# Kernel optimization log

Measured on AMD Instinct MI355X. Metric: run time of the kernel, lower is better.

The kernel has to match this reference:

```python
import jax, jax.numpy as jnp
import numpy as np

SEQ_LEN = 512
MAX_SPAN = 15
BATCH = 8
HIDDEN = 1024
WIDTH_DIM = 64
NUM_LABELS = 3


def _enumerate_spans(seq_len, max_span):
    starts, ends = [], []
    for s in range(seq_len):
        for e in range(s, min(s + max_span, seq_len)):
            starts.append(s)
            ends.append(e)
    return np.asarray(starts, np.int32), np.asarray(ends, np.int32)


def setup_inputs() -> dict:
    key = jax.random.key(0)
    k = jax.random.split(key, 6)
    starts, ends = _enumerate_spans(SEQ_LEN, MAX_SPAN)  # N = 7575
    d_in = HIDDEN * 2 + WIDTH_DIM  # 2112
    return {
        "sequence_output": jax.random.normal(k[0], (BATCH, SEQ_LEN, HIDDEN), jnp.float32),
        "width_emb": jax.random.normal(k[1], (MAX_SPAN, WIDTH_DIM), jnp.float32) * 0.02,
        "W1": jax.random.normal(k[2], (d_in, HIDDEN), jnp.float32) * (1.0 / np.sqrt(d_in)),
        "b1": jnp.zeros((HIDDEN,), jnp.float32),
        "W2": jax.random.normal(k[3], (HIDDEN, NUM_LABELS), jnp.float32) * (1.0 / np.sqrt(HIDDEN)),
        "b2": jnp.zeros((NUM_LABELS,), jnp.float32),
        "span_starts": jnp.asarray(starts),
        "span_ends": jnp.asarray(ends),
    }


def reference(sequence_output, width_emb, W1, b1, W2, b2, span_starts, span_ends):
    # Gather start/end token representations for every candidate span.
    B = sequence_output.shape[0]
    N = span_starts.shape[0]
    start_repr = sequence_output[:, span_starts]            # [B, N, H]
    end_repr = sequence_output[:, span_ends]                # [B, N, H]
    width_repr = width_emb[span_ends - span_starts]         # [N, 64]
    width_repr = jnp.broadcast_to(width_repr[None], (B, N, width_repr.shape[-1]))
    span_reprs = jnp.concatenate([start_repr, end_repr, width_repr], axis=-1)  # [B, N, 2H+64]
    # Span classifier MLP (dropout is identity in eval mode).
    h = jax.nn.relu(jnp.einsum("bnd,dh->bnh", span_reprs, W1) + b1)
    logits = jnp.einsum("bnh,hl->bnl", h, W2) + b2          # [B, N, num_labels]
    return logits
```

## Files before the change

kernel.cpp:

```cpp
#include <hip/hip_runtime.h>
#include <stdint.h>

#define SEQ 512
#define BATCH 8
#define HID 1024

typedef __attribute__((ext_vector_type(8))) __bf16 bf16x8;
typedef __attribute__((ext_vector_type(4))) float f32x4;

__device__ __forceinline__ unsigned short f2bf(float f) {
    unsigned int u = __float_as_uint(f);
    unsigned int r = 0x7fffu + ((u >> 16) & 1u);
    return (unsigned short)((u + r) >> 16);
}

__device__ __forceinline__ void unpack8(uint4 v, float* f) {
    f[0] = __uint_as_float(v.x << 16);
    f[1] = __uint_as_float(v.x & 0xffff0000u);
    f[2] = __uint_as_float(v.y << 16);
    f[3] = __uint_as_float(v.y & 0xffff0000u);
    f[4] = __uint_as_float(v.z << 16);
    f[5] = __uint_as_float(v.z & 0xffff0000u);
    f[6] = __uint_as_float(v.w << 16);
    f[7] = __uint_as_float(v.w & 0xffff0000u);
}

template <int CTRL>
__device__ __forceinline__ float dpp_add(float x) {
    int t = __builtin_amdgcn_update_dpp(0, __float_as_int(x), CTRL, 0xf, 0xf, true);
    return x + __int_as_float(t);
}
__device__ __forceinline__ float wave_sum63(float x) {
    x = dpp_add<0x111>(x);
    x = dpp_add<0x112>(x);
    x = dpp_add<0x114>(x);
    x = dpp_add<0x118>(x);
    x = dpp_add<0x142>(x);
    x = dpp_add<0x143>(x);
    return x;
}

__global__ __launch_bounds__(256) void k_prep(const float* __restrict__ seq,
                                              const float* __restrict__ wemb,
                                              const float* __restrict__ W1,
                                              const float* __restrict__ b1,
                                              const float* __restrict__ W2,
                                              ushort* __restrict__ seqb,
                                              ushort* __restrict__ Bt,
                                              ushort* __restrict__ Rbf,
                                              float* __restrict__ W2t) {
    __shared__ float tile[32][33];
    const int bid = blockIdx.x;
    const int tid = threadIdx.x;
    if (bid < 60) {
        int idx = bid * 256 + tid;
        int w = idx >> 10, j = idx & 1023;
        float a0 = b1[j], a1 = 0.f, a2 = 0.f, a3 = 0.f;
#pragma unroll
        for (int c = 0; c < 64; c += 4) {
            a0 = fmaf(wemb[w * 64 + c + 0], W1[(size_t)(2048 + c + 0) * 1024 + j], a0);
            a1 = fmaf(wemb[w * 64 + c + 1], W1[(size_t)(2048 + c + 1) * 1024 + j], a1);
            a2 = fmaf(wemb[w * 64 + c + 2], W1[(size_t)(2048 + c + 2) * 1024 + j], a2);
            a3 = fmaf(wemb[w * 64 + c + 3], W1[(size_t)(2048 + c + 3) * 1024 + j], a3);
        }
        Rbf[idx] = f2bf((a0 + a1) + (a2 + a3));
    } else if (bid < 72) {
        int idx = (bid - 60) * 256 + tid;
        int l = idx >> 10, j = idx & 1023;
        W2t[idx] = W2[j * 3 + l];
    } else if (bid < 4168) {
        int i = (bid - 72) * 256 + tid;
        float4 v = ((const float4*)seq)[i];
        ushort4 o;
        o.x = f2bf(v.x); o.y = f2bf(v.y); o.z = f2bf(v.z); o.w = f2bf(v.w);
        ((ushort4*)seqb)[i] = o;
    } else {
        int idx = bid - 4168;
        int nb = (idx & 63) * 32, kb = (idx >> 6) * 32;
        int tx = tid & 31, ty = tid >> 5;
        int n = nb + tx;
        int rb = (n < 1024) ? 0 : 1024;
        int nc = n - rb;
#pragma unroll
        for (int i = 0; i < 4; ++i) {
            int k = kb + ty + i * 8;
            tile[ty + i * 8][tx] = W1[(size_t)(rb + k) * 1024 + nc];
        }
        __syncthreads();
#pragma unroll
        for (int i = 0; i < 4; ++i) {
            int n2 = nb + ty + i * 8;
            Bt[(size_t)n2 * 1024 + kb + tx] = f2bf(tile[tx][ty + i * 8]);
        }
    }
}

__global__ __launch_bounds__(256) void k_gemm(const ushort* __restrict__ A,
                                              const ushort* __restrict__ Bt,
                                              ushort* __restrict__ P,
                                              ushort* __restrict__ Q) {
    __shared__ ushort Al[2][8192];
    __shared__ ushort Bl[2][8192];
    const int tid = threadIdx.x;
    const int wid = tid >> 6;
    const int lane = tid & 63;
    const int bid = blockIdx.x;
    const int x = bid & 7, t8 = bid >> 3;
    const int m0 = (((x >> 1) << 3) + (t8 >> 3)) * 128;
    const int n0 = (((x & 1) << 3) + (t8 & 7)) * 128;
    const int wm = (wid >> 1) * 64;
    const int wn = (wid & 1) * 64;
    const int srow = lane >> 2;
    const int scol = (lane & 3) * 8;
    const int fr = lane & 15;
    const int fk = (lane >> 4) * 8;

    f32x4 acc[4][4] = {};

    const ushort* Abase = A  + (size_t)(m0 + srow) * 1024 + scol;
    const ushort* Bbase = Bt + (size_t)(n0 + srow) * 1024 + scol;

#define STAGE(buf, k0)                                                                     \
    {                                                                                      \
        _Pragma("unroll")                                                                  \
        for (int r = 0; r < 4; ++r) {                                                      \
            int c = wid + 4 * r;                                                           \
            int half = c >> 3;                                                             \
            int rows = (c & 7) * 16;                                                       \
            const ushort* sa = Abase + (size_t)rows * 1024 + (k0) + half * 32;             \
            const ushort* sb = Bbase + (size_t)rows * 1024 + (k0) + half * 32;             \
            int loff = half * 4096 + rows * 32;                                            \
            __builtin_amdgcn_global_load_lds((const __attribute__((address_space(1))) void*)sa, \
                                             (__attribute__((address_space(3))) void*)(&Al[buf][loff]), \
                                             16, 0, 0);                                    \
            __builtin_amdgcn_global_load_lds((const __attribute__((address_space(1))) void*)sb, \
                                             (__attribute__((address_space(3))) void*)(&Bl[buf][loff]), \
                                             16, 0, 0);                                    \
        }                                                                                  \
    }

#define COMPUTE(cur)                                                                       \
    {                                                                                      \
        _Pragma("unroll")                                                                  \
        for (int kk = 0; kk < 2; ++kk) {                                                   \
            bf16x8 af[4], bg[4];                                                           \
            _Pragma("unroll")                                                              \
            for (int i = 0; i < 4; ++i)                                                    \
                af[i] = *(const bf16x8*)(&Al[cur][kk * 4096 + (wm + i * 16 + fr) * 32 + fk]); \
            _Pragma("unroll")                                                              \
            for (int j = 0; j < 4; ++j)                                                    \
                bg[j] = *(const bf16x8*)(&Bl[cur][kk * 4096 + (wn + j * 16 + fr) * 32 + fk]); \
            __builtin_amdgcn_s_setprio(1);                                                 \
            _Pragma("unroll")                                                              \
            for (int i = 0; i < 4; ++i)                                                    \
                _Pragma("unroll")                                                          \
                for (int j = 0; j < 4; ++j)                                                \
                    acc[i][j] = __builtin_amdgcn_mfma_f32_16x16x32_bf16(af[i], bg[j], acc[i][j], 0, 0, 0); \
            __builtin_amdgcn_s_setprio(0);                                                 \
        }                                                                                  \
    }

    STAGE(0, 0);
    for (int t = 0; t < 15; ++t) {
        const int cur = t & 1;
        STAGE(cur ^ 1, (t + 1) * 64);
        asm volatile("s_waitcnt vmcnt(8)" ::: "memory");
        __builtin_amdgcn_s_barrier();
        COMPUTE(cur);
        __builtin_amdgcn_s_barrier();
    }
    asm volatile("s_waitcnt vmcnt(0)" ::: "memory");
    __builtin_amdgcn_s_barrier();
    COMPUTE(1);
#undef STAGE
#undef COMPUTE

    ushort* Cb = (n0 < 1024) ? P : Q;
    const int nc0 = n0 & 1023;
    const int cr = (lane >> 4) * 4;
    const int cc = lane & 15;
#pragma unroll
    for (int i = 0; i < 4; ++i)
#pragma unroll
        for (int j = 0; j < 4; ++j) {
            ushort* Cp = Cb + (size_t)(m0 + wm + i * 16 + cr) * 1024 + (nc0 + wn + j * 16 + cc);
#pragma unroll
            for (int r = 0; r < 4; ++r)
                Cp[(size_t)r * 1024] = f2bf(acc[i][j][r]);
        }
}

__global__ __launch_bounds__(512, 2) void k_span6(const ushort* __restrict__ Pmat,
                                                  const ushort* __restrict__ Qmat,
                                                  const ushort* __restrict__ Rbf,
                                                  const float* __restrict__ W2t,
                                                  const float* __restrict__ b2,
                                                  float* __restrict__ out, int nspans) {
    __shared__ ushort Qs[22 * 1024];
    __shared__ ushort Rs[15 * 1024];
    const int tid = threadIdx.x;
    const int wid = tid >> 6, lane = tid & 63;
    const int b = blockIdx.x >> 6;
    const int s0 = (blockIdx.x & 63) << 3;

#pragma unroll
    for (int i = 0; i < 6; ++i) {
        int c = wid + (i << 3);
        if (c < 44) {
            int g = (c << 9) + lane * 8;
            int row = s0 + (g >> 10);
            if (row > SEQ - 1) row = SEQ - 1;
            const ushort* src = Qmat + (((size_t)(b << 9) + row) << 10) + (g & 1023);
            __builtin_amdgcn_global_load_lds((const __attribute__((address_space(1))) void*)src,
                                             (__attribute__((address_space(3))) void*)(Qs + (c << 9)),
                                             16, 0, 0);
        }
    }
#pragma unroll
    for (int i = 0; i < 4; ++i) {
        int c = wid + (i << 3);
        if (c < 30) {
            int g = (c << 9) + lane * 8;
            __builtin_amdgcn_global_load_lds((const __attribute__((address_space(1))) void*)(Rbf + g),
                                             (__attribute__((address_space(3))) void*)(Rs + (c << 9)),
                                             16, 0, 0);
        }
    }

    float w2r[3][2][8];
#pragma unroll
    for (int l = 0; l < 3; ++l)
#pragma unroll
        for (int it = 0; it < 2; ++it) {
            const float4* p = (const float4*)(W2t + l * 1024 + it * 512 + lane * 8);
            float4 v0 = p[0], v1 = p[1];
            w2r[l][it][0] = v0.x; w2r[l][it][1] = v0.y;
            w2r[l][it][2] = v0.z; w2r[l][it][3] = v0.w;
            w2r[l][it][4] = v1.x; w2r[l][it][5] = v1.y;
            w2r[l][it][6] = v1.z; w2r[l][it][7] = v1.w;
        }
    const float bb0 = b2[0], bb1 = b2[1], bb2 = b2[2];

    const int s = s0 + wid;
    float pf[16];
    {
        const uint4* pr = (const uint4*)(Pmat + (((size_t)(b << 9) + s) << 10) + lane * 8);
        unpack8(pr[0], pf);
        unpack8(pr[64], pf + 8);
    }

    __syncthreads();

    const int rrem = SEQ - s;
    const int nsp = (rrem < 15) ? rrem : 15;
    const int off = (rrem >= 15) ? 15 * s : (7575 - (rrem * (rrem + 1)) / 2);
    float* op = out + ((size_t)b * nspans + off) * 3;

    for (int w = 0; w < nsp; ++w) {
        const int erow = wid + w;
        float a0 = 0.f, a1 = 0.f, a2 = 0.f;
#pragma unroll
        for (int it = 0; it < 2; ++it) {
            uint4 qv = *(const uint4*)((const char*)Qs + erow * 2048 + it * 1024 + lane * 16);
            uint4 rv = *(const uint4*)((const char*)Rs + w * 2048 + it * 1024 + lane * 16);
            float qf[8], rf[8];
            unpack8(qv, qf);
            unpack8(rv, rf);
#pragma unroll
            for (int u = 0; u < 8; ++u) {
                float h = pf[it * 8 + u] + qf[u] + rf[u];
                h = fmaxf(h, 0.f);
                a0 = fmaf(h, w2r[0][it][u], a0);
                a1 = fmaf(h, w2r[1][it][u], a1);
                a2 = fmaf(h, w2r[2][it][u], a2);
            }
        }
        a0 = wave_sum63(a0);
        a1 = wave_sum63(a1);
        a2 = wave_sum63(a2);
        if (lane == 63) {
            op[w * 3 + 0] = a0 + bb0;
            op[w * 3 + 1] = a1 + bb1;
            op[w * 3 + 2] = a2 + bb2;
        }
    }
}

extern "C" void kernel_launch(void* const* d_in, const int* in_sizes, int n_in,
                              void* d_out, int out_size, void* d_ws, size_t ws_size,
                              hipStream_t stream) {
    const float* seq    = (const float*)d_in[0];
    const float* wemb   = (const float*)d_in[1];
    const float* W1     = (const float*)d_in[2];
    const float* b1     = (const float*)d_in[3];
    const float* W2     = (const float*)d_in[4];
    const float* b2     = (const float*)d_in[5];
    float* out = (float*)d_out;
    int nspans = in_sizes[6];

    char* ws = (char*)d_ws;
    ushort* seqb = (ushort*)ws;
    ushort* Bt   = (ushort*)(ws + (8u << 20));
    ushort* Pmat = (ushort*)(ws + (12u << 20));
    ushort* Qmat = (ushort*)(ws + (20u << 20));
    ushort* Rbf  = (ushort*)(ws + (28u << 20));
    float*  W2t  = (float*)(ws + (29u << 20));

    hipLaunchKernelGGL(k_prep, dim3(6216), dim3(256), 0, stream,
                       seq, wemb, W1, b1, W2, seqb, Bt, Rbf, W2t);
    hipLaunchKernelGGL(k_gemm, dim3(512), dim3(256), 0, stream, seqb, Bt, Pmat, Qmat);
    hipLaunchKernelGGL(k_span6, dim3(BATCH * 64), dim3(512), 0, stream,
                       Pmat, Qmat, Rbf, W2t, b2, out, nspans);
}
```

Before: 54.53 us.

## Stream Q rows from global with register prefetch, keep R in fp32, pack FMA math

```diff
diff --git a/kernel.cpp b/kernel.cpp
--- a/kernel.cpp
+++ b/kernel.cpp
@@ -7,6 +7,7 @@
 
 typedef __attribute__((ext_vector_type(8))) __bf16 bf16x8;
 typedef __attribute__((ext_vector_type(4))) float f32x4;
+typedef __attribute__((ext_vector_type(2))) float f32x2;
 
 __device__ __forceinline__ unsigned short f2bf(float f) {
     unsigned int u = __float_as_uint(f);
@@ -25,6 +26,13 @@
     f[7] = __uint_as_float(v.w & 0xffff0000u);
 }
 
+__device__ __forceinline__ f32x2 up2(unsigned int v) {
+    f32x2 r;
+    r.x = __uint_as_float(v << 16);
+    r.y = __uint_as_float(v & 0xffff0000u);
+    return r;
+}
+
 template <int CTRL>
 __device__ __forceinline__ float dpp_add(float x) {
     int t = __builtin_amdgcn_update_dpp(0, __float_as_int(x), CTRL, 0xf, 0xf, true);
@@ -47,7 +55,7 @@
                                               const float* __restrict__ W2,
                                               ushort* __restrict__ seqb,
                                               ushort* __restrict__ Bt,
-                                              ushort* __restrict__ Rbf,
+                                              float* __restrict__ Rf,
                                               float* __restrict__ W2t) {
     __shared__ float tile[32][33];
     const int bid = blockIdx.x;
@@ -63,7 +71,7 @@
             a2 = fmaf(wemb[w * 64 + c + 2], W1[(size_t)(2048 + c + 2) * 1024 + j], a2);
             a3 = fmaf(wemb[w * 64 + c + 3], W1[(size_t)(2048 + c + 3) * 1024 + j], a3);
         }
-        Rbf[idx] = f2bf((a0 + a1) + (a2 + a3));
+        Rf[idx] = (a0 + a1) + (a2 + a3);
     } else if (bid < 72) {
         int idx = (bid - 60) * 256 + tid;
         int l = idx >> 10, j = idx & 1023;
@@ -190,63 +198,50 @@
         }
 }
 
-__global__ __launch_bounds__(512, 2) void k_span6(const ushort* __restrict__ Pmat,
+__global__ __launch_bounds__(512, 2) void k_span8(const ushort* __restrict__ Pmat,
                                                   const ushort* __restrict__ Qmat,
-                                                  const ushort* __restrict__ Rbf,
+                                                  const float* __restrict__ Rf,
                                                   const float* __restrict__ W2t,
                                                   const float* __restrict__ b2,
                                                   float* __restrict__ out, int nspans) {
-    __shared__ ushort Qs[22 * 1024];
-    __shared__ ushort Rs[15 * 1024];
+    __shared__ float Rs[15 * 1024];
     const int tid = threadIdx.x;
     const int wid = tid >> 6, lane = tid & 63;
     const int b = blockIdx.x >> 6;
     const int s0 = (blockIdx.x & 63) << 3;
 
 #pragma unroll
-    for (int i = 0; i < 6; ++i) {
+    for (int i = 0; i < 8; ++i) {
         int c = wid + (i << 3);
-        if (c < 44) {
-            int g = (c << 9) + lane * 8;
-            int row = s0 + (g >> 10);
-            if (row > SEQ - 1) row = SEQ - 1;
-            const ushort* src = Qmat + (((size_t)(b << 9) + row) << 10) + (g & 1023);
-            __builtin_amdgcn_global_load_lds((const __attribute__((address_space(1))) void*)src,
-                                             (__attribute__((address_space(3))) void*)(Qs + (c << 9)),
+        if (c < 60) {
+            int g = (c << 8) + lane * 4;
+            __builtin_amdgcn_global_load_lds((const __attribute__((address_space(1))) void*)(Rf + g),
+                                             (__attribute__((address_space(3))) void*)(Rs + g),
                                              16, 0, 0);
         }
     }
-#pragma unroll
-    for (int i = 0; i < 4; ++i) {
-        int c = wid + (i << 3);
-        if (c < 30) {
-            int g = (c << 9) + lane * 8;
-            __builtin_amdgcn_global_load_lds((const __attribute__((address_space(1))) void*)(Rbf + g),
-                                             (__attribute__((address_space(3))) void*)(Rs + (c << 9)),
-                                             16, 0, 0);
-        }
-    }
-
-    float w2r[3][2][8];
+
+    f32x2 w2r2[3][2][4];
 #pragma unroll
     for (int l = 0; l < 3; ++l)
 #pragma unroll
         for (int it = 0; it < 2; ++it) {
             const float4* p = (const float4*)(W2t + l * 1024 + it * 512 + lane * 8);
             float4 v0 = p[0], v1 = p[1];
-            w2r[l][it][0] = v0.x; w2r[l][it][1] = v0.y;
-            w2r[l][it][2] = v0.z; w2r[l][it][3] = v0.w;
-            w2r[l][it][4] = v1.x; w2r[l][it][5] = v1.y;
-            w2r[l][it][6] = v1.z; w2r[l][it][7] = v1.w;
+            w2r2[l][it][0] = (f32x2){v0.x, v0.y};
+            w2r2[l][it][1] = (f32x2){v0.z, v0.w};
+            w2r2[l][it][2] = (f32x2){v1.x, v1.y};
+            w2r2[l][it][3] = (f32x2){v1.z, v1.w};
         }
     const float bb0 = b2[0], bb1 = b2[1], bb2 = b2[2];
 
     const int s = s0 + wid;
-    float pf[16];
+    f32x2 pf2[8];
     {
         const uint4* pr = (const uint4*)(Pmat + (((size_t)(b << 9) + s) << 10) + lane * 8);
-        unpack8(pr[0], pf);
-        unpack8(pr[64], pf + 8);
+        uint4 p0 = pr[0], p1 = pr[64];
+        pf2[0] = up2(p0.x); pf2[1] = up2(p0.y); pf2[2] = up2(p0.z); pf2[3] = up2(p0.w);
+        pf2[4] = up2(p1.x); pf2[5] = up2(p1.y); pf2[6] = up2(p1.z); pf2[7] = up2(p1.w);
     }
 
     __syncthreads();
@@ -256,25 +251,39 @@
     const int off = (rrem >= 15) ? 15 * s : (7575 - (rrem * (rrem + 1)) / 2);
     float* op = out + ((size_t)b * nspans + off) * 3;
 
+    const uint4* qp = (const uint4*)(Qmat + (((size_t)(b << 9) + s) << 10) + lane * 8);
+    uint4 q0 = qp[0], q1 = qp[64];
+
     for (int w = 0; w < nsp; ++w) {
-        const int erow = wid + w;
-        float a0 = 0.f, a1 = 0.f, a2 = 0.f;
+        uint4 nq0, nq1;
+        if (w + 1 < nsp) {
+            qp += 128;
+            nq0 = qp[0]; nq1 = qp[64];
+        } else {
+            nq0 = q0; nq1 = q1;
+        }
+        f32x2 A0 = {0.f, 0.f}, A1 = {0.f, 0.f}, A2 = {0.f, 0.f};
 #pragma unroll
         for (int it = 0; it < 2; ++it) {
-            uint4 qv = *(const uint4*)((const char*)Qs + erow * 2048 + it * 1024 + lane * 16);
-            uint4 rv = *(const uint4*)((const char*)Rs + w * 2048 + it * 1024 + lane * 16);
-            float qf[8], rf[8];
-            unpack8(qv, qf);
-            unpack8(rv, rf);
-#pragma unroll
-            for (int u = 0; u < 8; ++u) {
-                float h = pf[it * 8 + u] + qf[u] + rf[u];
-                h = fmaxf(h, 0.f);
-                a0 = fmaf(h, w2r[0][it][u], a0);
-                a1 = fmaf(h, w2r[1][it][u], a1);
-                a2 = fmaf(h, w2r[2][it][u], a2);
+            uint4 qv = (it == 0) ? q0 : q1;
+            const float4* rp = (const float4*)(Rs + w * 1024 + it * 512 + lane * 8);
+            float4 ra = rp[0], rb = rp[1];
+            f32x2 q2[4] = {up2(qv.x), up2(qv.y), up2(qv.z), up2(qv.w)};
+            f32x2 r2[4] = {(f32x2){ra.x, ra.y}, (f32x2){ra.z, ra.w},
+                           (f32x2){rb.x, rb.y}, (f32x2){rb.z, rb.w}};
+#pragma unroll
+            for (int k = 0; k < 4; ++k) {
+                f32x2 h = pf2[it * 4 + k] + q2[k] + r2[k];
+                h.x = fmaxf(h.x, 0.f);
+                h.y = fmaxf(h.y, 0.f);
+                A0 += h * w2r2[0][it][k];
+                A1 += h * w2r2[1][it][k];
+                A2 += h * w2r2[2][it][k];
             }
         }
+        float a0 = A0.x + A0.y;
+        float a1 = A1.x + A1.y;
+        float a2 = A2.x + A2.y;
         a0 = wave_sum63(a0);
         a1 = wave_sum63(a1);
         a2 = wave_sum63(a2);
@@ -283,6 +292,7 @@
             op[w * 3 + 1] = a1 + bb1;
             op[w * 3 + 2] = a2 + bb2;
         }
+        q0 = nq0; q1 = nq1;
     }
 }
 
@@ -303,12 +313,12 @@
     ushort* Bt   = (ushort*)(ws + (8u << 20));
     ushort* Pmat = (ushort*)(ws + (12u << 20));
     ushort* Qmat = (ushort*)(ws + (20u << 20));
-    ushort* Rbf  = (ushort*)(ws + (28u << 20));
+    float*  Rf   = (float*)(ws + (28u << 20));
     float*  W2t  = (float*)(ws + (29u << 20));
 
     hipLaunchKernelGGL(k_prep, dim3(6216), dim3(256), 0, stream,
-                       seq, wemb, W1, b1, W2, seqb, Bt, Rbf, W2t);
+                       seq, wemb, W1, b1, W2, seqb, Bt, Rf, W2t);
     hipLaunchKernelGGL(k_gemm, dim3(512), dim3(256), 0, stream, seqb, Bt, Pmat, Qmat);
-    hipLaunchKernelGGL(k_span6, dim3(BATCH * 64), dim3(512), 0, stream,
-                       Pmat, Qmat, Rbf, W2t, b2, out, nspans);
-}
+    hipLaunchKernelGGL(k_span8, dim3(BATCH * 64), dim3(512), 0, stream,
+                       Pmat, Qmat, Rf, W2t, b2, out, nspans);
+}
```

Result: no change. 53.64 us (-1.6%).
